# Kernel optimization log

Measured on AMD Instinct MI355X. Metric: run time of the kernel, lower is better.

## Reference

```python
import jax, jax.numpy as jnp
import numpy as np

TEMPERATURE = 0.5
EPS = 1e-8  # torch CosineSimilarity default eps


def setup_inputs() -> dict:
    key = jax.random.key(0)
    k1, k2 = jax.random.split(key)
    N, D = 4096, 256
    return {
        "batch_embeddings": jax.random.normal(k1, (N, D), dtype=jnp.float32),
        "batch_augmented_embeddings": jax.random.normal(k2, (N, D), dtype=jnp.float32),
    }


def reference(batch_embeddings, batch_augmented_embeddings):
    N = batch_embeddings.shape[0]
    emb = jnp.concatenate([batch_embeddings, batch_augmented_embeddings], axis=0)  # (2N, D)
    # cosine similarity = normalized dot products (normalize + GEMM rewrite of the
    # broadcasted nn.CosineSimilarity)
    norms = jnp.sqrt(jnp.sum(emb * emb, axis=-1, keepdims=True))
    emb_n = emb / jnp.maximum(norms, EPS)
    sim = jnp.einsum("id,jd->ij", emb_n, emb_n) / TEMPERATURE  # (2N, 2N)
    # negative mask: (~eye(N)).repeat(2,2) -> False where (i mod N) == (j mod N)
    idx = jnp.arange(2 * N)
    neg_mask = (idx[:, None] % N) != (idx[None, :] % N)
    exp_sim = jnp.exp(sim) * neg_mask.astype(sim.dtype)
    sum_exp = jnp.sum(exp_sim, axis=-1)  # (2N,)
    pos = jnp.arange(N)
    positive_sim = sim[pos, N + pos]  # (N,)
    negative_sim_sum = sum_exp[:N]  # (N,)
    loss = -jnp.mean(jnp.log(jnp.exp(positive_sim) / negative_sim_sum))
    return loss
```

## Files before the change

kernel.cpp:

```cpp
#include <hip/hip_runtime.h>
#include <hip/hip_bf16.h>

#define NROWS 4096
#define DDIM  256
#define EPS   1e-8f
#define SCALE 1.69864944f
#define LN2   0.69314718056f

#define NJ 32
#define JS 256
#define BT 64
#define CH (JS / BT)
#define BUFSH (4 * 8 * 64 * 8)

typedef __attribute__((ext_vector_type(8))) short short8;
typedef __attribute__((ext_vector_type(4))) float f32x4;

#if __has_builtin(__builtin_amdgcn_exp2f)
#define EXP2F(x) __builtin_amdgcn_exp2f(x)
#else
#define EXP2F(x) exp2f(x)
#endif

__device__ __forceinline__ unsigned short f2bf(float x) {
    union { __hip_bfloat16 h; unsigned short u; } c;
    c.h = __float2bfloat16(x);
    return c.u;
}

__global__ void normalize_kernel(const float* __restrict__ a,
                                 const float* __restrict__ b,
                                 unsigned short* __restrict__ en,
                                 float* __restrict__ S, int N) {
    const int wave = threadIdx.x >> 6, lane = threadIdx.x & 63;
    const int row = blockIdx.x * 4 + wave;
    const float* src = (row < N) ? (a + (size_t)row * DDIM)
                                 : (b + (size_t)(row - N) * DDIM);
    const float4 v = reinterpret_cast<const float4*>(src)[lane];
    float ss = v.x * v.x + v.y * v.y + v.z * v.z + v.w * v.w;
    #pragma unroll
    for (int off = 32; off > 0; off >>= 1) ss += __shfl_xor(ss, off);
    const float inv = SCALE / fmaxf(sqrtf(ss), EPS * SCALE);
    ushort4 o;
    o.x = f2bf(v.x * inv);
    o.y = f2bf(v.y * inv);
    o.z = f2bf(v.z * inv);
    o.w = f2bf(v.w * inv);
    *reinterpret_cast<ushort4*>(en + (size_t)row * DDIM + lane * 4) = o;
    if (lane == 0 && row < N) S[row] = 0.0f;
}

__global__ __launch_bounds__(256, 2) void simsum_kernel(
        const short* __restrict__ en,
        float* __restrict__ S,
        float* __restrict__ pos) {
    __shared__ short bt[2 * BUFSH];
    const int tid = threadIdx.x;
    const int wave = tid >> 6, lane = tid & 63;
    const int lrow = lane & 15, quad = lane >> 4;
    const int i0 = blockIdx.x * 256 + wave * 64;
    const int jb = blockIdx.y * JS;

    short8 afrag[4][8];
    #pragma unroll
    for (int t = 0; t < 4; ++t)
        #pragma unroll
        for (int ks = 0; ks < 8; ++ks)
            afrag[t][ks] = *reinterpret_cast<const short8*>(
                en + (size_t)(i0 + t * 16 + lrow) * DDIM + ks * 32 + quad * 8);

    float rowsum[4][4];
    #pragma unroll
    for (int t = 0; t < 4; ++t)
        #pragma unroll
        for (int r = 0; r < 4; ++r) rowsum[t][r] = 0.0f;

    auto stage = [&](int jc, int buf) {
        const short* g = en + (size_t)(jc + wave * 16 + lrow) * DDIM + quad * 8;
        short* l = bt + buf * BUFSH + wave * 4096;
        #pragma unroll
        for (int ks = 0; ks < 8; ++ks) {
            __builtin_amdgcn_global_load_lds(
                (const __attribute__((address_space(1))) void*)(g + ks * 32),
                (__attribute__((address_space(3))) void*)(l + ks * 512),
                16, 0, 0);
        }
    };

    stage(jb, 0);
    for (int c = 0; c < CH; ++c) {
        __syncthreads();
        if (c + 1 < CH) stage(jb + (c + 1) * BT, (c + 1) & 1);
        const short* lb = bt + (c & 1) * BUFSH;
        #pragma unroll
        for (int cg = 0; cg < 4; ++cg) {
            f32x4 acc[4];
            #pragma unroll
            for (int t = 0; t < 4; ++t) acc[t] = f32x4{0.f, 0.f, 0.f, 0.f};
            #pragma unroll
            for (int ks = 0; ks < 8; ++ks) {
                const short8 bfrag = *reinterpret_cast<const short8*>(
                    lb + cg * 4096 + ks * 512 + lane * 8);
                #pragma unroll
                for (int t = 0; t < 4; ++t)
                    acc[t] = __builtin_amdgcn_mfma_f32_16x16x32_bf16(
                        afrag[t][ks], bfrag, acc[t], 0, 0, 0);
            }
            const int col = jb + c * BT + cg * 16 + lrow;
            const int cm = col & (NROWS - 1);
            #pragma unroll
            for (int t = 0; t < 4; ++t) {
                #pragma unroll
                for (int r = 0; r < 4; ++r)
                    rowsum[t][r] += EXP2F(acc[t][r]);
                const unsigned delta = (unsigned)(cm - (i0 + t * 16 + quad * 4));
                if (delta < 4u) {
                    const float d = (delta == 0) ? acc[t][0]
                                  : (delta == 1) ? acc[t][1]
                                  : (delta == 2) ? acc[t][2]
                                  :                acc[t][3];
                    const float ed = EXP2F(d);
                    #pragma unroll
                    for (int r = 0; r < 4; ++r)
                        if (r == (int)delta) rowsum[t][r] -= ed;
                    if (col >= NROWS) pos[cm] = d * LN2;
                }
            }
        }
    }

    #pragma unroll
    for (int t = 0; t < 4; ++t) {
        #pragma unroll
        for (int r = 0; r < 4; ++r) {
            float v = rowsum[t][r];
            v += __shfl_xor(v, 1);
            v += __shfl_xor(v, 2);
            v += __shfl_xor(v, 4);
            v += __shfl_xor(v, 8);
            rowsum[t][r] = v;
        }
        if (lrow < 4) {
            const float v = (lrow == 0) ? rowsum[t][0]
                          : (lrow == 1) ? rowsum[t][1]
                          : (lrow == 2) ? rowsum[t][2]
                          :               rowsum[t][3];
            atomicAdd(&S[i0 + t * 16 + quad * 4 + lrow], v);
        }
    }
}

__global__ void loss_kernel(const float* __restrict__ S,
                            const float* __restrict__ pos,
                            float* __restrict__ out, int N) {
    float acc = 0.0f;
    for (int i = threadIdx.x; i < N; i += 1024)
        acc += pos[i] - __logf(S[i]);
    #pragma unroll
    for (int off = 32; off > 0; off >>= 1) acc += __shfl_xor(acc, off);
    __shared__ float wsum[16];
    const int wave = threadIdx.x >> 6, lane = threadIdx.x & 63;
    if (lane == 0) wsum[wave] = acc;
    __syncthreads();
    if (threadIdx.x == 0) {
        float tot = 0.0f;
        #pragma unroll
        for (int w = 0; w < 16; ++w) tot += wsum[w];
        out[0] = -tot / (float)N;
    }
}

extern "C" void kernel_launch(void* const* d_in, const int* in_sizes, int n_in,
                              void* d_out, int out_size, void* d_ws, size_t ws_size,
                              hipStream_t stream) {
    const float* a = (const float*)d_in[0];
    const float* b = (const float*)d_in[1];
    float* out = (float*)d_out;
    const int N = NROWS;

    char* ws = (char*)d_ws;
    unsigned short* en = (unsigned short*)ws;
    float* S = (float*)(ws + (size_t)2 * N * DDIM * sizeof(unsigned short));
    float* pos = S + N;

    normalize_kernel<<<(2 * N) / 4, 256, 0, stream>>>(a, b, en, S, N);
    simsum_kernel<<<dim3(N / 256, NJ), 256, 0, stream>>>((const short*)en, S, pos);
    loss_kernel<<<1, 1024, 0, stream>>>(S, pos, out, N);
}
```

Before: 88.48 us.

## Move diagonal and positive-pair handling out of GEMM loop into parallel loss kernel

Drops the per-tile diagonal and positive-pair detection from the simsum inner loop, so the hot path only accumulates exp2 of every similarity. The loss kernel now recomputes the self and positive dot products from the bf16 normalized rows, subtracts their exp2 terms from the row sums, and runs across 64 blocks that finish through an atomic accumulator and completion counter. It also issues the first LDS stage before the A-fragment loads so they overlap. The subtraction happens in fp32 after accumulation, so the computed dot products may differ slightly from the MFMA values they cancel, which is a small numerical risk.

New measurement: 106.2 us. +20.0%, slower.

```diff
diff --git a/kernel.cpp b/kernel.cpp
--- a/kernel.cpp
+++ b/kernel.cpp
@@ -27,11 +27,18 @@
     c.h = __float2bfloat16(x);
     return c.u;
 }
+__device__ __forceinline__ float bf2f(unsigned short u) {
+    union { unsigned int i; float f; } c;
+    c.i = ((unsigned int)u) << 16;
+    return c.f;
+}
 
 __global__ void normalize_kernel(const float* __restrict__ a,
                                  const float* __restrict__ b,
                                  unsigned short* __restrict__ en,
-                                 float* __restrict__ S, int N) {
+                                 float* __restrict__ S,
+                                 float* __restrict__ cell,
+                                 unsigned int* __restrict__ counter, int N) {
     const int wave = threadIdx.x >> 6, lane = threadIdx.x & 63;
     const int row = blockIdx.x * 4 + wave;
     const float* src = (row < N) ? (a + (size_t)row * DDIM)
@@ -48,12 +55,12 @@
     o.w = f2bf(v.w * inv);
     *reinterpret_cast<ushort4*>(en + (size_t)row * DDIM + lane * 4) = o;
     if (lane == 0 && row < N) S[row] = 0.0f;
+    if (blockIdx.x == 0 && threadIdx.x == 0) { *cell = 0.0f; *counter = 0u; }
 }
 
 __global__ __launch_bounds__(256, 2) void simsum_kernel(
         const short* __restrict__ en,
-        float* __restrict__ S,
-        float* __restrict__ pos) {
+        float* __restrict__ S) {
     __shared__ short bt[2 * BUFSH];
     const int tid = threadIdx.x;
     const int wave = tid >> 6, lane = tid & 63;
@@ -61,20 +68,6 @@
     const int i0 = blockIdx.x * 256 + wave * 64;
     const int jb = blockIdx.y * JS;
 
-    short8 afrag[4][8];
-    #pragma unroll
-    for (int t = 0; t < 4; ++t)
-        #pragma unroll
-        for (int ks = 0; ks < 8; ++ks)
-            afrag[t][ks] = *reinterpret_cast<const short8*>(
-                en + (size_t)(i0 + t * 16 + lrow) * DDIM + ks * 32 + quad * 8);
-
-    float rowsum[4][4];
-    #pragma unroll
-    for (int t = 0; t < 4; ++t)
-        #pragma unroll
-        for (int r = 0; r < 4; ++r) rowsum[t][r] = 0.0f;
-
     auto stage = [&](int jc, int buf) {
         const short* g = en + (size_t)(jc + wave * 16 + lrow) * DDIM + quad * 8;
         short* l = bt + buf * BUFSH + wave * 4096;
@@ -88,6 +81,21 @@
     };
 
     stage(jb, 0);
+
+    short8 afrag[4][8];
+    #pragma unroll
+    for (int t = 0; t < 4; ++t)
+        #pragma unroll
+        for (int ks = 0; ks < 8; ++ks)
+            afrag[t][ks] = *reinterpret_cast<const short8*>(
+                en + (size_t)(i0 + t * 16 + lrow) * DDIM + ks * 32 + quad * 8);
+
+    float rowsum[4][4];
+    #pragma unroll
+    for (int t = 0; t < 4; ++t)
+        #pragma unroll
+        for (int r = 0; r < 4; ++r) rowsum[t][r] = 0.0f;
+
     for (int c = 0; c < CH; ++c) {
         __syncthreads();
         if (c + 1 < CH) stage(jb + (c + 1) * BT, (c + 1) & 1);
@@ -106,26 +114,11 @@
                     acc[t] = __builtin_amdgcn_mfma_f32_16x16x32_bf16(
                         afrag[t][ks], bfrag, acc[t], 0, 0, 0);
             }
-            const int col = jb + c * BT + cg * 16 + lrow;
-            const int cm = col & (NROWS - 1);
             #pragma unroll
-            for (int t = 0; t < 4; ++t) {
+            for (int t = 0; t < 4; ++t)
                 #pragma unroll
                 for (int r = 0; r < 4; ++r)
                     rowsum[t][r] += EXP2F(acc[t][r]);
-                const unsigned delta = (unsigned)(cm - (i0 + t * 16 + quad * 4));
-                if (delta < 4u) {
-                    const float d = (delta == 0) ? acc[t][0]
-                                  : (delta == 1) ? acc[t][1]
-                                  : (delta == 2) ? acc[t][2]
-                                  :                acc[t][3];
-                    const float ed = EXP2F(d);
-                    #pragma unroll
-                    for (int r = 0; r < 4; ++r)
-                        if (r == (int)delta) rowsum[t][r] -= ed;
-                    if (col >= NROWS) pos[cm] = d * LN2;
-                }
-            }
         }
     }
 
@@ -150,23 +143,48 @@
     }
 }
 
-__global__ void loss_kernel(const float* __restrict__ S,
-                            const float* __restrict__ pos,
+__global__ void loss_kernel(const unsigned short* __restrict__ en,
+                            const float* __restrict__ S,
+                            float* __restrict__ cell,
+                            unsigned int* __restrict__ counter,
                             float* __restrict__ out, int N) {
-    float acc = 0.0f;
-    for (int i = threadIdx.x; i < N; i += 1024)
-        acc += pos[i] - __logf(S[i]);
-    #pragma unroll
-    for (int off = 32; off > 0; off >>= 1) acc += __shfl_xor(acc, off);
-    __shared__ float wsum[16];
-    const int wave = threadIdx.x >> 6, lane = threadIdx.x & 63;
-    if (lane == 0) wsum[wave] = acc;
+    const int tid = threadIdx.x;
+    const int wave = tid >> 6, lane = tid & 63;
+    const int gw = blockIdx.x * 4 + wave;
+    float wacc = 0.0f;
+    for (int rr = 0; rr < 16; ++rr) {
+        const int row = gw * 16 + rr;
+        const ushort4 ua = *reinterpret_cast<const ushort4*>(
+            en + (size_t)row * DDIM + lane * 4);
+        const ushort4 ub = *reinterpret_cast<const ushort4*>(
+            en + (size_t)(N + row) * DDIM + lane * 4);
+        const float a0 = bf2f(ua.x), a1 = bf2f(ua.y),
+                    a2 = bf2f(ua.z), a3 = bf2f(ua.w);
+        const float b0 = bf2f(ub.x), b1 = bf2f(ub.y),
+                    b2 = bf2f(ub.z), b3 = bf2f(ub.w);
+        float sd = a0 * a0 + a1 * a1 + a2 * a2 + a3 * a3;
+        float pd = a0 * b0 + a1 * b1 + a2 * b2 + a3 * b3;
+        #pragma unroll
+        for (int off = 32; off > 0; off >>= 1) {
+            sd += __shfl_xor(sd, off);
+            pd += __shfl_xor(pd, off);
+        }
+        if (lane == 0) {
+            const float Sc = S[row] - EXP2F(sd) - EXP2F(pd);
+            wacc += pd * LN2 - LN2 * __log2f(Sc);
+        }
+    }
+    __shared__ float bs[4];
+    if (lane == 0) bs[wave] = wacc;
     __syncthreads();
-    if (threadIdx.x == 0) {
-        float tot = 0.0f;
-        #pragma unroll
-        for (int w = 0; w < 16; ++w) tot += wsum[w];
-        out[0] = -tot / (float)N;
+    if (tid == 0) {
+        atomicAdd(cell, bs[0] + bs[1] + bs[2] + bs[3]);
+        __threadfence();
+        const unsigned int old = atomicAdd(counter, 1u);
+        if (old == gridDim.x - 1) {
+            const float tot = atomicAdd(cell, 0.0f);
+            out[0] = -tot / (float)N;
+        }
     }
 }
 
@@ -181,9 +199,11 @@
     char* ws = (char*)d_ws;
     unsigned short* en = (unsigned short*)ws;
     float* S = (float*)(ws + (size_t)2 * N * DDIM * sizeof(unsigned short));
-    float* pos = S + N;
-
-    normalize_kernel<<<(2 * N) / 4, 256, 0, stream>>>(a, b, en, S, N);
-    simsum_kernel<<<dim3(N / 256, NJ), 256, 0, stream>>>((const short*)en, S, pos);
-    loss_kernel<<<1, 1024, 0, stream>>>(S, pos, out, N);
-}
+    float* cell = S + N;
+    unsigned int* counter = (unsigned int*)(cell + 1);
+
+    normalize_kernel<<<(2 * N) / 4, 256, 0, stream>>>(a, b, en, S, cell,
+                                                      counter, N);
+    simsum_kernel<<<dim3(N / 256, NJ), 256, 0, stream>>>((const short*)en, S);
+    loss_kernel<<<64, 256, 0, stream>>>(en, S, cell, counter, out, N);
+}
```
